# Performance work log

Measured on AMD Instinct MI355X. Metric: run time of the kernel, lower is better.

Reference implementation:

```python
import jax, jax.numpy as jnp
import numpy as np

EPS = 1e-12  # F.normalize eps
NEG_SLOPE = 0.01  # F.leaky_relu default


def _neigh_agg(x, edge_index, W, b, num_node):
    # x: [N_src, d]; edge_index: [2, E]; W: [d, d]; b: [d]
    src, tgt = edge_index[0], edge_index[1]
    h = jax.nn.relu(x @ W + b)                      # [N_src, d]
    gathered = h[tgt]                               # [E, d] irregular gather
    aggr = jax.ops.segment_sum(gathered, src, num_segments=num_node)  # [N, d]
    deg = jax.ops.segment_sum(jnp.ones_like(src, dtype=aggr.dtype), src,
                              num_segments=num_node)
    deg = jnp.clip(deg, 1.0, None)
    return aggr / deg[:, None]                      # mean-aggregate; dropout is eval no-op


def setup_inputs() -> dict:
    key = jax.random.key(0)
    ks = jax.random.split(key, 16)
    N, E, d = 50000, 800000, 128
    f = lambda k, s: jax.random.normal(k, s, dtype=jnp.float32)
    inp = {
        "x_r": f(ks[0], (N, d)),
        "x_u": f(ks[1], (N, d)),
        "x_b": f(ks[2], (N, d)),
        "x_node": f(ks[3], (N, d)),
        "edges_r": jax.random.randint(ks[4], (2, E), 0, N),
        "edges_u": jax.random.randint(ks[5], (2, E), 0, N),
        "edges_b": jax.random.randint(ks[6], (2, E), 0, N),
        "num_node": N,
        # learned params (Linear weights stored as [in, out])
        "W_r": f(ks[7], (d, d)) * 0.05, "b_r": f(ks[8], (d,)) * 0.05,
        "W_u": f(ks[9], (d, d)) * 0.05, "b_u": f(ks[10], (d,)) * 0.05,
        "W_b": f(ks[11], (d, d)) * 0.05, "b_b": f(ks[12], (d,)) * 0.05,
        "u": f(ks[13], (2 * d, 1)),
        "W_lin": f(ks[14], (2 * d, d)) * 0.05, "b_lin": f(ks[15], (d,)) * 0.05,
    }
    return inp


def reference(x_r, x_u, x_b, x_node, edges_r, edges_u, edges_b, num_node,
              W_r, b_r, W_u, b_u, W_b, b_b, u, W_lin, b_lin):
    r_aggr = _neigh_agg(x_r, edges_r, W_r, b_r, num_node)  # [N, d]
    u_aggr = _neigh_agg(x_u, edges_u, W_u, b_u, num_node)
    b_aggr = _neigh_agg(x_b, edges_b, W_b, b_b, num_node)

    def score(aggr):
        cat = jnp.concatenate([aggr, x_node], axis=-1)      # [N, 2d]
        return jnp.exp(jax.nn.leaky_relu(cat @ u, NEG_SLOPE))  # [N, 1]

    r_s, u_s, b_s = score(r_aggr), score(u_aggr), score(b_aggr)
    denom = r_s + u_s + b_s
    combined = (r_s / denom) * r_aggr + (u_s / denom) * u_aggr + (b_s / denom) * b_aggr
    combined = jnp.concatenate([x_node, combined], axis=-1)  # [N, 2d]
    h = jax.nn.relu(combined @ W_lin + b_lin)                # [N, d]
    norm = jnp.maximum(jnp.linalg.norm(h, axis=-1, keepdims=True), EPS)
    return h / norm
```

## Files before the change

### kernel.cpp

```cpp
#include <hip/hip_runtime.h>

typedef unsigned int uint_t;

#define NPB 120
#define NBMAX 512
#define CAP 16
#define TILE 4096
#define NFILL 192
#define CAPP 4096

__device__ __forceinline__ float bflo(unsigned int u) {
  union { unsigned int i; float f; } v; v.i = u << 16; return v.f;
}
__device__ __forceinline__ float bfhi(unsigned int u) {
  union { unsigned int i; float f; } v; v.i = u & 0xffff0000u; return v.f;
}
__device__ __forceinline__ unsigned short f2bf(float f) {
  union { float f; unsigned int i; } v; v.f = f;
  unsigned int u = v.i;
  return (unsigned short)((u + 0x7fffu + ((u >> 16) & 1u)) >> 16);
}
__device__ __forceinline__ unsigned int pack2bf(float a, float b) {
  return (unsigned int)f2bf(a) | ((unsigned int)f2bf(b) << 16);
}

__device__ __forceinline__ void gemm_role(
    const float* __restrict__ x, const float* __restrict__ W,
    const float* __restrict__ bb, unsigned short* __restrict__ hg,
    int N, int bx, float* xs) {
  int tid = threadIdx.x;
  long row0 = (long)bx * 32;
  const float4* xv = (const float4*)x;
  for (int idx = tid; idx < 1024; idx += 256) {
    int r = idx >> 5, k4 = idx & 31;
    long row = row0 + r;
    float4 v = (row < N) ? xv[row * 32 + k4] : make_float4(0.f, 0.f, 0.f, 0.f);
    *(float4*)&xs[r * 128 + k4 * 4] = v;
  }
  __syncthreads();
  int w = tid >> 6, lane = tid & 63;
  int r0 = w * 8;
  int c = lane * 2;
  float b0 = bb[c], b1 = bb[c + 1];
  float acc[8][2];
#pragma unroll
  for (int i = 0; i < 8; ++i) { acc[i][0] = b0; acc[i][1] = b1; }
  const float2* Wp = (const float2*)W;
  float2 wq[4];
#pragma unroll
  for (int kk = 0; kk < 4; ++kk) wq[kk] = Wp[kk * 64 + lane];
  for (int k = 0; k < 128; k += 4) {
    float4 xr[8];
#pragma unroll
    for (int i = 0; i < 8; ++i) xr[i] = *(const float4*)&xs[(r0 + i) * 128 + k];
    float2 wn[4];
#pragma unroll
    for (int kk = 0; kk < 4; ++kk) wn[kk] = wq[kk];
    if (k + 4 < 128) {
#pragma unroll
      for (int kk = 0; kk < 4; ++kk) wn[kk] = Wp[(k + 4 + kk) * 64 + lane];
    }
#pragma unroll
    for (int kk = 0; kk < 4; ++kk) {
#pragma unroll
      for (int i = 0; i < 8; ++i) {
        float xv_ = ((const float*)&xr[i])[kk];
        acc[i][0] += xv_ * wq[kk].x;
        acc[i][1] += xv_ * wq[kk].y;
      }
    }
#pragma unroll
    for (int kk = 0; kk < 4; ++kk) wq[kk] = wn[kk];
  }
#pragma unroll
  for (int i = 0; i < 8; ++i) {
    long row = row0 + r0 + i;
    if (row < N) {
      float v0 = fmaxf(acc[i][0], 0.f), v1 = fmaxf(acc[i][1], 0.f);
      *(uint_t*)&hg[row * 128 + c] = pack2bf(v0, v1);
    }
  }
}

__global__ __launch_bounds__(256) void phase1_kernel(
    const float* __restrict__ x0, const float* __restrict__ W0,
    const float* __restrict__ b0, const int* __restrict__ e0,
    const int* __restrict__ e1, const int* __restrict__ e2,
    int* __restrict__ bcnt, unsigned short* __restrict__ h,
    int N, int E, int nbG) {
  __shared__ __align__(16) char smem[16384];
  int bid = blockIdx.x;
  if (bid >= NFILL) {
    gemm_role(x0, W0, b0, h, N, bid - NFILL, (float*)smem);
    return;
  }
  int g = bid >> 6, chunk = bid & 63;
  const int* edges = (g == 0) ? e0 : (g == 1) ? e1 : e2;
  int NB = (N + NPB - 1) / NPB;
  int* lh = (int*)smem;
  for (int i = threadIdx.x; i < NB; i += 256) lh[i] = 0;
  __syncthreads();
  int per = (E + 63) >> 6;
  int beg = chunk * per;
  int end = beg + per; if (end > E) end = E;
  for (int e = beg + threadIdx.x; e < end; e += 256) {
    int b = edges[e] / NPB;
    atomicAdd(&lh[b], 1);
  }
  __syncthreads();
  int* cnt = bcnt + (size_t)g * NB;
  for (int i = threadIdx.x; i < NB; i += 256)
    if (lh[i]) atomicAdd(&cnt[i], lh[i]);
}

__global__ __launch_bounds__(1024) void scan3_kernel(
    const int* __restrict__ counts, int* __restrict__ row_start,
    int* __restrict__ cursor, int N) {
  int g = blockIdx.x;
  const int* cnt = counts + (size_t)g * N;
  int* rs  = row_start + (size_t)g * N;
  int* cur = cursor + (size_t)g * N;
  __shared__ int wsum[16];
  int tid = threadIdx.x;
  int lane = tid & 63, wv = tid >> 6;
  int chunk = (N + 1023) / 1024;
  int begin = tid * chunk;
  int end = begin + chunk; if (end > N) end = N;
  int s = 0;
  for (int i = begin; i < end; ++i) s += cnt[i];
  int incl = s;
  for (int off = 1; off < 64; off <<= 1) {
    int t = __shfl_up(incl, off, 64);
    if (lane >= off) incl += t;
  }
  if (lane == 63) wsum[wv] = incl;
  __syncthreads();
  if (wv == 0) {
    int ws = (lane < 16) ? wsum[lane] : 0;
    int wincl = ws;
    for (int off = 1; off < 16; off <<= 1) {
      int t = __shfl_up(wincl, off, 64);
      if (lane >= off) wincl += t;
    }
    if (lane < 16) wsum[lane] = wincl - ws;
  }
  __syncthreads();
  int base = wsum[wv] + (incl - s);
  for (int i = begin; i < end; ++i) {
    rs[i] = base;
    cur[i] = base;
    base += cnt[i];
  }
}

__global__ __launch_bounds__(256) void phase2_kernel(
    const float* __restrict__ x1, const float* __restrict__ x2,
    const float* __restrict__ W1, const float* __restrict__ W2,
    const float* __restrict__ b1, const float* __restrict__ b2,
    const int* __restrict__ e0, const int* __restrict__ e1,
    const int* __restrict__ e2, int* __restrict__ bcur,
    uint_t* __restrict__ gout, unsigned short* __restrict__ h,
    int N, int E, int nbG) {
  __shared__ __align__(16) char smem[CAP * NBMAX * 4 + NBMAX * 4];
  int bid = blockIdx.x;
  if (bid >= NFILL) {
    int bx = bid - NFILL;
    int g = (bx < nbG) ? 1 : 2;
    int b2x = (bx < nbG) ? bx : bx - nbG;
    gemm_role((g == 1) ? x1 : x2, (g == 1) ? W1 : W2, (g == 1) ? b1 : b2,
              h + (size_t)g * N * 128, N, b2x, (float*)smem);
    return;
  }
  int g = bid >> 6, chunk = bid & 63;
  const int* edges = (g == 0) ? e0 : (g == 1) ? e1 : e2;
  int NB = (N + NPB - 1) / NPB;
  uint_t* stage = (uint_t*)smem;
  int* scnt = (int*)(smem + CAP * NBMAX * 4);
  int* cur = bcur + (size_t)g * NB;
  uint_t* out = gout + (size_t)g * E;
  for (int i = threadIdx.x; i < NB; i += 256) scnt[i] = 0;
  __syncthreads();
  int per = (E + 63) >> 6;
  int beg = chunk * per;
  int end = beg + per; if (end > E) end = E;
  for (int t0 = beg; t0 < end; t0 += TILE) {
    int t1 = t0 + TILE; if (t1 > end) t1 = end;
    for (int e = t0 + threadIdx.x; e < t1; e += 256) {
      int src = edges[e], tgt = edges[E + e];
      int b = src / NPB;
      uint_t pair = ((uint_t)(src - b * NPB) << 16) | (uint_t)tgt;
      int idx = atomicAdd(&scnt[b], 1);
      if (idx < CAP) stage[b * CAP + idx] = pair;
      else out[atomicAdd(&cur[b], 1)] = pair;
    }
    __syncthreads();
    for (int b = threadIdx.x; b < NB; b += 256) {
      int c = scnt[b];
      if (c) {
        if (c > CAP) c = CAP;
        int base = atomicAdd(&cur[b], c);
        for (int i = 0; i < c; ++i) out[base + i] = stage[b * CAP + i];
        scnt[b] = 0;
      }
    }
    __syncthreads();
  }
}

__global__ __launch_bounds__(256) void agg_bucket_kernel(
    const int* __restrict__ bstart, const int* __restrict__ bcnt,
    const uint_t* __restrict__ gout, const unsigned short* __restrict__ h,
    unsigned short* __restrict__ aggr, int N, int E) {
  __shared__ uint_t sorted[CAPP];
  __shared__ int hcnt[NPB];
  __shared__ int hoff[NPB + 1];
  __shared__ int hfill[NPB];
  int g = blockIdx.y, b = blockIdx.x;
  int NB = gridDim.x;
  int tid = threadIdx.x, w = tid >> 6, lane = tid & 63;
  for (int i = tid; i < NPB; i += 256) hcnt[i] = 0;
  __syncthreads();
  int beg = bstart[(size_t)g * NB + b];
  int cnt = bcnt[(size_t)g * NB + b];
  if (cnt > CAPP) cnt = CAPP;
  const uint_t* pr = gout + (size_t)g * E + beg;
  for (int i = tid; i < cnt; i += 256) atomicAdd(&hcnt[pr[i] >> 16], 1);
  __syncthreads();
  if (w == 0) {
    int i0 = lane * 2, i1 = lane * 2 + 1;
    int v0 = (i0 < NPB) ? hcnt[i0] : 0;
    int v1 = (i1 < NPB) ? hcnt[i1] : 0;
    int s = v0 + v1;
    int incl = s;
    for (int off = 1; off < 64; off <<= 1) {
      int t = __shfl_up(incl, off, 64);
      if (lane >= off) incl += t;
    }
    int excl = incl - s;
    if (i0 < NPB) { hoff[i0] = excl; hfill[i0] = excl; }
    if (i1 < NPB) { hoff[i1] = excl + v0; hfill[i1] = excl + v0; }
    if (lane == 63) hoff[NPB] = incl;
  }
  __syncthreads();
  for (int i = tid; i < cnt; i += 256) {
    uint_t p = pr[i];
    int slot = atomicAdd(&hfill[p >> 16], 1);
    sorted[slot] = p;
  }
  __syncthreads();
  const uint_t* hb = (const uint_t*)(h + (size_t)g * N * 128);
  uint_t* ab = (uint_t*)(aggr + (size_t)g * N * 128);
  long nb0 = (long)b * NPB;
  for (int r = w; r < NPB; r += 4) {
    long node = nb0 + r;
    if (node >= N) break;
    int s = hoff[r], e = hoff[r + 1];
    int deg = e - s;
    float a0 = 0.f, a1 = 0.f;
    if (deg > 0) {
      for (int j = 0; j < deg; j += 8) {
        int t[8]; uint_t v[8];
#pragma unroll
        for (int q = 0; q < 8; ++q) {
          int idx = j + q; if (idx >= deg) idx = deg - 1;
          t[q] = (int)(sorted[s + idx] & 0xffffu);
        }
#pragma unroll
        for (int q = 0; q < 8; ++q) v[q] = hb[(size_t)t[q] * 64 + lane];
        int m = deg - j; if (m > 8) m = 8;
#pragma unroll
        for (int q = 0; q < 8; ++q)
          if (q < m) { a0 += bflo(v[q]); a1 += bfhi(v[q]); }
      }
    }
    float idg = 1.f / (float)(deg > 1 ? deg : 1);
    ab[node * 64 + lane] = pack2bf(a0 * idg, a1 * idg);
  }
}

__global__ __launch_bounds__(256) void combine_final_kernel(
    const unsigned short* __restrict__ aggr, const float* __restrict__ x_node,
    const float* __restrict__ u, const float* __restrict__ W,
    const float* __restrict__ b, float* __restrict__ out, int N) {
  __shared__ float xs[32][256];
  int tid = threadIdx.x;
  long row0 = (long)blockIdx.x * 32;
  const float4* xv = (const float4*)x_node;
  for (int idx = tid; idx < 1024; idx += 256) {
    int r = idx >> 5, k4 = idx & 31;
    long row = row0 + r;
    float4 v = (row < N) ? xv[row * 32 + k4] : make_float4(0.f, 0.f, 0.f, 0.f);
    *(float4*)&xs[r][k4 * 4] = v;
  }
  __syncthreads();

  int w = tid >> 6, lane = tid & 63;
  int r0 = w * 8;
  const uint_t* ap = (const uint_t*)aggr;
  float2 ua = ((const float2*)u)[lane];
  float2 ux = ((const float2*)u)[64 + lane];
#pragma unroll
  for (int i = 0; i < 8; ++i) {
    int r = r0 + i;
    long n = row0 + r;
    float c0 = 0.f, c1 = 0.f;
    if (n < N) {
      uint_t vr = ap[n * 64 + lane];
      uint_t vu = ap[((size_t)N + n) * 64 + lane];
      uint_t vb = ap[((size_t)2 * N + n) * 64 + lane];
      float ar0 = bflo(vr), ar1 = bfhi(vr);
      float au0 = bflo(vu), au1 = bfhi(vu);
      float ab0 = bflo(vb), ab1 = bfhi(vb);
      float2 xn = *(const float2*)&xs[r][lane * 2];
      float pr = ua.x * ar0 + ua.y * ar1;
      float pu = ua.x * au0 + ua.y * au1;
      float pb = ua.x * ab0 + ua.y * ab1;
      float px = ux.x * xn.x + ux.y * xn.y;
      for (int m = 32; m >= 1; m >>= 1) {
        pr += __shfl_xor(pr, m, 64);
        pu += __shfl_xor(pu, m, 64);
        pb += __shfl_xor(pb, m, 64);
        px += __shfl_xor(px, m, 64);
      }
      float zr = pr + px, zu = pu + px, zb = pb + px;
      zr = zr > 0.f ? zr : 0.01f * zr;
      zu = zu > 0.f ? zu : 0.01f * zu;
      zb = zb > 0.f ? zb : 0.01f * zb;
      float sr = expf(zr), su = expf(zu), sb = expf(zb);
      float inv = 1.f / (sr + su + sb);
      float wr = sr * inv, wu = su * inv, wb = sb * inv;
      c0 = wr * ar0 + wu * au0 + wb * ab0;
      c1 = wr * ar1 + wu * au1 + wb * ab1;
    }
    float2 cc; cc.x = c0; cc.y = c1;
    *(float2*)&xs[r][128 + lane * 2] = cc;
  }
  __syncthreads();

  int c = lane * 2;
  float b0 = b[c], b1 = b[c + 1];
  float acc[8][2];
#pragma unroll
  for (int i = 0; i < 8; ++i) { acc[i][0] = b0; acc[i][1] = b1; }
  const float2* Wp = (const float2*)W;
  float2 wq[4];
#pragma unroll
  for (int kk = 0; kk < 4; ++kk) wq[kk] = Wp[kk * 64 + lane];
  for (int k = 0; k < 256; k += 4) {
    float4 xr[8];
#pragma unroll
    for (int i = 0; i < 8; ++i) xr[i] = *(const float4*)&xs[r0 + i][k];
    float2 wn[4];
#pragma unroll
    for (int kk = 0; kk < 4; ++kk) wn[kk] = wq[kk];
    if (k + 4 < 256) {
#pragma unroll
      for (int kk = 0; kk < 4; ++kk) wn[kk] = Wp[(k + 4 + kk) * 64 + lane];
    }
#pragma unroll
    for (int kk = 0; kk < 4; ++kk) {
#pragma unroll
      for (int i = 0; i < 8; ++i) {
        float xv_ = ((const float*)&xr[i])[kk];
        acc[i][0] += xv_ * wq[kk].x;
        acc[i][1] += xv_ * wq[kk].y;
      }
    }
#pragma unroll
    for (int kk = 0; kk < 4; ++kk) wq[kk] = wn[kk];
  }
#pragma unroll
  for (int i = 0; i < 8; ++i) {
    float v0 = fmaxf(acc[i][0], 0.f), v1 = fmaxf(acc[i][1], 0.f);
    float ss = v0 * v0 + v1 * v1;
    for (int m = 32; m >= 1; m >>= 1) ss += __shfl_xor(ss, m, 64);
    float inv = 1.f / fmaxf(sqrtf(ss), 1e-12f);
    long row = row0 + r0 + i;
    if (row < N) {
      float2 o; o.x = v0 * inv; o.y = v1 * inv;
      *(float2*)&out[row * 128 + c] = o;
    }
  }
}

extern "C" void kernel_launch(void* const* d_in, const int* in_sizes, int n_in,
                              void* d_out, int out_size, void* d_ws, size_t ws_size,
                              hipStream_t stream) {
  const float* x_r    = (const float*)d_in[0];
  const float* x_u    = (const float*)d_in[1];
  const float* x_b    = (const float*)d_in[2];
  const float* x_node = (const float*)d_in[3];
  const int* e_r = (const int*)d_in[4];
  const int* e_u = (const int*)d_in[5];
  const int* e_b = (const int*)d_in[6];
  const float* W_r   = (const float*)d_in[8];
  const float* b_r   = (const float*)d_in[9];
  const float* W_u   = (const float*)d_in[10];
  const float* b_u   = (const float*)d_in[11];
  const float* W_b   = (const float*)d_in[12];
  const float* b_b   = (const float*)d_in[13];
  const float* u     = (const float*)d_in[14];
  const float* W_lin = (const float*)d_in[15];
  const float* b_lin = (const float*)d_in[16];

  int N = in_sizes[0] / 128;
  int E = in_sizes[4] / 2;
  int NB = (N + NPB - 1) / NPB;

  unsigned short* aggr = (unsigned short*)d_ws;
  unsigned short* h = aggr + (size_t)3 * N * 128;
  uint_t* gout = (uint_t*)(h + (size_t)3 * N * 128);
  int* bcnt   = (int*)(gout + (size_t)3 * E);
  int* bstart = bcnt + (size_t)3 * NB;
  int* bcur   = bstart + (size_t)3 * NB;

  hipMemsetAsync(bcnt, 0, (size_t)3 * NB * sizeof(int), stream);

  dim3 blk(256);
  int nbG = (N + 31) / 32;
  dim3 gP1(NFILL + nbG);
  dim3 gP2(NFILL + 2 * nbG);
  dim3 gAgg(NB, 3);
  dim3 gFinal((N + 31) / 32);

  phase1_kernel<<<gP1, blk, 0, stream>>>(x_r, W_r, b_r, e_r, e_u, e_b,
                                         bcnt, h, N, E, nbG);
  scan3_kernel<<<3, 1024, 0, stream>>>(bcnt, bstart, bcur, NB);
  phase2_kernel<<<gP2, blk, 0, stream>>>(x_u, x_b, W_u, W_b, b_u, b_b,
                                         e_r, e_u, e_b, bcur, gout, h,
                                         N, E, nbG);
  agg_bucket_kernel<<<gAgg, blk, 0, stream>>>(bstart, bcnt, gout, h,
                                              aggr, N, E);
  combine_final_kernel<<<gFinal, blk, 0, stream>>>(aggr, x_node, u, W_lin,
                                                   b_lin, (float*)d_out, N);
}
```

Before: 451.3 us.

## Split aggregation buckets across two blocks, shrink LDS, drop GEMM shared staging

The aggregation kernel now launches two blocks per bucket, each handling half the nodes. Both blocks load the bucket's edge list into LDS once and filter it by node range, which doubles parallelism and cuts per-block LDS. Phase-2 staging shrinks (CAP 12, TILE 2048, bucket array sized to 420) to lower LDS use. The GEMM role now streams x rows straight from global memory into registers instead of staging them in shared memory. The costs are each bucket's edge list being read twice, more register pressure in the GEMM, and silently dropped edges if a bucket exceeds the new caps.

Result: slower. 596.4 us (+32.2%).

```diff
diff --git a/kernel.cpp b/kernel.cpp
--- a/kernel.cpp
+++ b/kernel.cpp
@@ -3,11 +3,14 @@
 typedef unsigned int uint_t;
 
 #define NPB 120
-#define NBMAX 512
-#define CAP 16
-#define TILE 4096
+#define NSPL 2
+#define NPS (NPB / NSPL)
+#define NBQ 420
+#define CAP 12
+#define TILE 2048
 #define NFILL 192
-#define CAPP 4096
+#define RAWCAP 2560
+#define SRTCAP 1536
 
 __device__ __forceinline__ float bflo(unsigned int u) {
   union { unsigned int i; float f; } v; v.i = u << 16; return v.f;
@@ -27,54 +30,60 @@
 __device__ __forceinline__ void gemm_role(
     const float* __restrict__ x, const float* __restrict__ W,
     const float* __restrict__ bb, unsigned short* __restrict__ hg,
-    int N, int bx, float* xs) {
+    int N, int bx) {
   int tid = threadIdx.x;
-  long row0 = (long)bx * 32;
-  const float4* xv = (const float4*)x;
-  for (int idx = tid; idx < 1024; idx += 256) {
-    int r = idx >> 5, k4 = idx & 31;
-    long row = row0 + r;
-    float4 v = (row < N) ? xv[row * 32 + k4] : make_float4(0.f, 0.f, 0.f, 0.f);
-    *(float4*)&xs[r * 128 + k4 * 4] = v;
-  }
-  __syncthreads();
   int w = tid >> 6, lane = tid & 63;
-  int r0 = w * 8;
+  long row0 = (long)bx * 32 + w * 8;
   int c = lane * 2;
   float b0 = bb[c], b1 = bb[c + 1];
   float acc[8][2];
 #pragma unroll
   for (int i = 0; i < 8; ++i) { acc[i][0] = b0; acc[i][1] = b1; }
+  const float4* xv = (const float4*)x;
   const float2* Wp = (const float2*)W;
+  int rbase[8];
+#pragma unroll
+  for (int i = 0; i < 8; ++i) {
+    long r = row0 + i;
+    if (r > (long)N - 1) r = (long)N - 1;
+    rbase[i] = (int)(r * 32);
+  }
+  float4 xq[8];
   float2 wq[4];
 #pragma unroll
+  for (int i = 0; i < 8; ++i) xq[i] = xv[rbase[i]];
+#pragma unroll
   for (int kk = 0; kk < 4; ++kk) wq[kk] = Wp[kk * 64 + lane];
-  for (int k = 0; k < 128; k += 4) {
-    float4 xr[8];
-#pragma unroll
-    for (int i = 0; i < 8; ++i) xr[i] = *(const float4*)&xs[(r0 + i) * 128 + k];
+  for (int q = 0; q < 32; ++q) {
+    float4 xn[8];
     float2 wn[4];
 #pragma unroll
+    for (int i = 0; i < 8; ++i) xn[i] = xq[i];
+#pragma unroll
     for (int kk = 0; kk < 4; ++kk) wn[kk] = wq[kk];
-    if (k + 4 < 128) {
-#pragma unroll
-      for (int kk = 0; kk < 4; ++kk) wn[kk] = Wp[(k + 4 + kk) * 64 + lane];
+    if (q < 31) {
+#pragma unroll
+      for (int i = 0; i < 8; ++i) xn[i] = xv[rbase[i] + q + 1];
+#pragma unroll
+      for (int kk = 0; kk < 4; ++kk) wn[kk] = Wp[(q * 4 + 4 + kk) * 64 + lane];
     }
 #pragma unroll
     for (int kk = 0; kk < 4; ++kk) {
 #pragma unroll
       for (int i = 0; i < 8; ++i) {
-        float xv_ = ((const float*)&xr[i])[kk];
+        float xv_ = ((const float*)&xq[i])[kk];
         acc[i][0] += xv_ * wq[kk].x;
         acc[i][1] += xv_ * wq[kk].y;
       }
     }
 #pragma unroll
+    for (int i = 0; i < 8; ++i) xq[i] = xn[i];
+#pragma unroll
     for (int kk = 0; kk < 4; ++kk) wq[kk] = wn[kk];
   }
 #pragma unroll
   for (int i = 0; i < 8; ++i) {
-    long row = row0 + r0 + i;
+    long row = row0 + i;
     if (row < N) {
       float v0 = fmaxf(acc[i][0], 0.f), v1 = fmaxf(acc[i][1], 0.f);
       *(uint_t*)&hg[row * 128 + c] = pack2bf(v0, v1);
@@ -88,16 +97,15 @@
     const int* __restrict__ e1, const int* __restrict__ e2,
     int* __restrict__ bcnt, unsigned short* __restrict__ h,
     int N, int E, int nbG) {
-  __shared__ __align__(16) char smem[16384];
+  __shared__ int lh[NBQ];
   int bid = blockIdx.x;
   if (bid >= NFILL) {
-    gemm_role(x0, W0, b0, h, N, bid - NFILL, (float*)smem);
+    gemm_role(x0, W0, b0, h, N, bid - NFILL);
     return;
   }
   int g = bid >> 6, chunk = bid & 63;
   const int* edges = (g == 0) ? e0 : (g == 1) ? e1 : e2;
   int NB = (N + NPB - 1) / NPB;
-  int* lh = (int*)smem;
   for (int i = threadIdx.x; i < NB; i += 256) lh[i] = 0;
   __syncthreads();
   int per = (E + 63) >> 6;
@@ -161,21 +169,20 @@
     const int* __restrict__ e2, int* __restrict__ bcur,
     uint_t* __restrict__ gout, unsigned short* __restrict__ h,
     int N, int E, int nbG) {
-  __shared__ __align__(16) char smem[CAP * NBMAX * 4 + NBMAX * 4];
+  __shared__ uint_t stage[CAP * NBQ];
+  __shared__ int scnt[NBQ];
   int bid = blockIdx.x;
   if (bid >= NFILL) {
     int bx = bid - NFILL;
     int g = (bx < nbG) ? 1 : 2;
     int b2x = (bx < nbG) ? bx : bx - nbG;
     gemm_role((g == 1) ? x1 : x2, (g == 1) ? W1 : W2, (g == 1) ? b1 : b2,
-              h + (size_t)g * N * 128, N, b2x, (float*)smem);
+              h + (size_t)g * N * 128, N, b2x);
     return;
   }
   int g = bid >> 6, chunk = bid & 63;
   const int* edges = (g == 0) ? e0 : (g == 1) ? e1 : e2;
   int NB = (N + NPB - 1) / NPB;
-  uint_t* stage = (uint_t*)smem;
-  int* scnt = (int*)(smem + CAP * NBMAX * 4);
   int* cur = bcur + (size_t)g * NB;
   uint_t* out = gout + (size_t)g * E;
   for (int i = threadIdx.x; i < NB; i += 256) scnt[i] = 0;
@@ -210,68 +217,71 @@
 __global__ __launch_bounds__(256) void agg_bucket_kernel(
     const int* __restrict__ bstart, const int* __restrict__ bcnt,
     const uint_t* __restrict__ gout, const unsigned short* __restrict__ h,
-    unsigned short* __restrict__ aggr, int N, int E) {
-  __shared__ uint_t sorted[CAPP];
-  __shared__ int hcnt[NPB];
-  __shared__ int hoff[NPB + 1];
-  __shared__ int hfill[NPB];
-  int g = blockIdx.y, b = blockIdx.x;
-  int NB = gridDim.x;
+    unsigned short* __restrict__ aggr, int N, int E, int NB) {
+  __shared__ uint_t raw[RAWCAP];
+  __shared__ uint_t sorted[SRTCAP];
+  __shared__ int hcnt[NPS];
+  __shared__ int hoff[NPS + 1];
+  __shared__ int hfill[NPS];
+  int g = blockIdx.y;
+  int bb = blockIdx.x;
+  int b = bb >> 1, half = bb & 1;
+  int lo = half * NPS;
   int tid = threadIdx.x, w = tid >> 6, lane = tid & 63;
-  for (int i = tid; i < NPB; i += 256) hcnt[i] = 0;
-  __syncthreads();
+  for (int i = tid; i < NPS; i += 256) hcnt[i] = 0;
   int beg = bstart[(size_t)g * NB + b];
   int cnt = bcnt[(size_t)g * NB + b];
-  if (cnt > CAPP) cnt = CAPP;
+  if (cnt > RAWCAP) cnt = RAWCAP;
   const uint_t* pr = gout + (size_t)g * E + beg;
-  for (int i = tid; i < cnt; i += 256) atomicAdd(&hcnt[pr[i] >> 16], 1);
+  for (int i = tid; i < cnt; i += 256) raw[i] = pr[i];
+  __syncthreads();
+  for (int i = tid; i < cnt; i += 256) {
+    int rel = (int)(raw[i] >> 16) - lo;
+    if ((unsigned)rel < (unsigned)NPS) atomicAdd(&hcnt[rel], 1);
+  }
   __syncthreads();
   if (w == 0) {
-    int i0 = lane * 2, i1 = lane * 2 + 1;
-    int v0 = (i0 < NPB) ? hcnt[i0] : 0;
-    int v1 = (i1 < NPB) ? hcnt[i1] : 0;
-    int s = v0 + v1;
-    int incl = s;
+    int v = (lane < NPS) ? hcnt[lane] : 0;
+    int incl = v;
     for (int off = 1; off < 64; off <<= 1) {
       int t = __shfl_up(incl, off, 64);
       if (lane >= off) incl += t;
     }
-    int excl = incl - s;
-    if (i0 < NPB) { hoff[i0] = excl; hfill[i0] = excl; }
-    if (i1 < NPB) { hoff[i1] = excl + v0; hfill[i1] = excl + v0; }
-    if (lane == 63) hoff[NPB] = incl;
+    if (lane < NPS) { hoff[lane] = incl - v; hfill[lane] = incl - v; }
+    if (lane == NPS - 1) hoff[NPS] = incl;
   }
   __syncthreads();
   for (int i = tid; i < cnt; i += 256) {
-    uint_t p = pr[i];
-    int slot = atomicAdd(&hfill[p >> 16], 1);
-    sorted[slot] = p;
-  }
-  __syncthreads();
-  const uint_t* hb = (const uint_t*)(h + (size_t)g * N * 128);
+    uint_t p = raw[i];
+    int rel = (int)(p >> 16) - lo;
+    if ((unsigned)rel < (unsigned)NPS) {
+      int slot = atomicAdd(&hfill[rel], 1);
+      if (slot < SRTCAP) sorted[slot] = p & 0xffffu;
+    }
+  }
+  __syncthreads();
+  const uint_t* hb = (const uint_t*)(h + (size_t)g * N * 128) + lane;
   uint_t* ab = (uint_t*)(aggr + (size_t)g * N * 128);
-  long nb0 = (long)b * NPB;
-  for (int r = w; r < NPB; r += 4) {
+  long nb0 = (long)b * NPB + lo;
+  for (int r = w; r < NPS; r += 4) {
     long node = nb0 + r;
     if (node >= N) break;
     int s = hoff[r], e = hoff[r + 1];
     int deg = e - s;
     float a0 = 0.f, a1 = 0.f;
-    if (deg > 0) {
-      for (int j = 0; j < deg; j += 8) {
-        int t[8]; uint_t v[8];
-#pragma unroll
-        for (int q = 0; q < 8; ++q) {
-          int idx = j + q; if (idx >= deg) idx = deg - 1;
-          t[q] = (int)(sorted[s + idx] & 0xffffu);
-        }
-#pragma unroll
-        for (int q = 0; q < 8; ++q) v[q] = hb[(size_t)t[q] * 64 + lane];
-        int m = deg - j; if (m > 8) m = 8;
-#pragma unroll
-        for (int q = 0; q < 8; ++q)
-          if (q < m) { a0 += bflo(v[q]); a1 += bfhi(v[q]); }
+    for (int j = 0; j < deg; j += 8) {
+      uint_t off[8], v[8];
+#pragma unroll
+      for (int q = 0; q < 8; ++q) {
+        int idx = j + q; if (idx >= deg) idx = deg - 1;
+        off[q] = sorted[s + idx] << 6;
       }
+#pragma unroll
+      for (int q = 0; q < 8; ++q) v[q] = hb[off[q]];
+      int m = deg - j; if (m > 8) m = 8;
+#pragma unroll
+      for (int q = 0; q < 8; ++q)
+        if (q < m) { a0 += bflo(v[q]); a1 += bfhi(v[q]); }
     }
     float idg = 1.f / (float)(deg > 1 ? deg : 1);
     ab[node * 64 + lane] = pack2bf(a0 * idg, a1 * idg);
@@ -420,7 +430,7 @@
   int nbG = (N + 31) / 32;
   dim3 gP1(NFILL + nbG);
   dim3 gP2(NFILL + 2 * nbG);
-  dim3 gAgg(NB, 3);
+  dim3 gAgg(NB * NSPL, 3);
   dim3 gFinal((N + 31) / 32);
 
   phase1_kernel<<<gP1, blk, 0, stream>>>(x_r, W_r, b_r, e_r, e_u, e_b,
@@ -430,7 +440,7 @@
                                          e_r, e_u, e_b, bcur, gout, h,
                                          N, E, nbG);
   agg_bucket_kernel<<<gAgg, blk, 0, stream>>>(bstart, bcnt, gout, h,
-                                              aggr, N, E);
+                                              aggr, N, E, NB);
   combine_final_kernel<<<gFinal, blk, 0, stream>>>(aggr, x_node, u, W_lin,
                                                    b_lin, (float*)d_out, N);
 }
```
